# Kernel tuning notes

Hardware: AMD Instinct MI355X
Metric: run time of the kernel (lower is better)

## Reference

```python
import jax, jax.numpy as jnp
import numpy as np

B, G, K = 16, 5000, 256
NUM_CELLS, HID = 100, 64
STEPS, ALPHA = 10, 0.1


def setup_inputs() -> dict:
    key = jax.random.key(0)
    ks = jax.random.split(key, 10)
    ctl = jax.random.normal(ks[0], (B, G), dtype=jnp.float32)
    drug_targets = jax.random.uniform(ks[1], (B, G), dtype=jnp.float32)
    cell_idx = jax.random.randint(ks[2], (B,), 0, NUM_CELLS)
    drug_fp = jax.random.normal(ks[3], (B, 128), dtype=jnp.float32)
    # gene->module membership matrix (constructor constant M_gk)
    M = jax.random.uniform(ks[4], (G, K), dtype=jnp.float32)
    # module-module adjacency (constructor constant A_kk), column-normalized for stability
    A = jax.random.uniform(ks[5], (K, K), dtype=jnp.float32)
    A = A / jnp.sum(A, axis=0, keepdims=True)
    # shared Dense(hidden_dim, relu): input feature dim is 3 (ctl, t, z_gene stacked)
    W1 = jax.random.normal(ks[6], (3, HID), dtype=jnp.float32) * 0.5
    b1 = jnp.zeros((HID,), dtype=jnp.float32)
    cell_emb = jax.random.normal(ks[7], (NUM_CELLS, HID), dtype=jnp.float32) * 0.05
    W2 = jax.random.normal(ks[8], (HID, 1), dtype=jnp.float32) * 0.1
    b2 = jnp.zeros((1,), dtype=jnp.float32)
    return {"ctl": ctl, "drug_targets": drug_targets, "cell_idx": cell_idx,
            "drug_fp": drug_fp, "M": M, "A": A, "W1": W1, "b1": b1,
            "cell_emb": cell_emb, "W2": W2, "b2": b2}


def reference(ctl, drug_targets, cell_idx, drug_fp, M, A, W1, b1, cell_emb, W2, b2):
    t = drug_targets                                   # [B, G]
    # max-pool gene targets into modules: max_g t[b,g] * M[g,k]
    t_mod = jnp.max(t[:, :, None] * M[None, :, :], axis=1)   # [B, K]
    # APPNP propagation: Z = (1-alpha) * Z @ A + alpha * S, fixed 10 steps
    Z = t_mod
    for _ in range(STEPS):
        Z = (1.0 - ALPHA) * (Z @ A) + ALPHA * t_mod
    z_gene = Z @ M.T                                   # [B, G]
    x = jnp.stack([ctl, t, z_gene], axis=-1)           # [B, G, 3]
    h = jax.nn.relu(x @ W1 + b1)                       # [B, G, HID]
    h = h + cell_emb[cell_idx][:, None, :]             # broadcast cell embedding
    y = jnp.squeeze(h @ W2 + b2, axis=-1)              # [B, G]
    return y
```

## Files before the change

kernel.cpp:

```cpp
#include <hip/hip_runtime.h>

#define G 5000
#define K 256
#define BATCH 16
#define HID 64
#define STEPS 10
#define NC 125
#define GPER 40

__global__ void maxpool_kernel(const float* __restrict__ t,
                               const float* __restrict__ M,
                               float* __restrict__ partials) {
    __shared__ float4 tl[GPER];
    const int c   = blockIdx.x % NC;
    const int bg  = blockIdx.x / NC;
    const int tid = threadIdx.x;
    const int g0  = c * GPER;
    const int b0  = bg * 4;

    if (tid < GPER) {
        int g = g0 + tid;
        tl[tid] = make_float4(t[(b0 + 0) * G + g], t[(b0 + 1) * G + g],
                              t[(b0 + 2) * G + g], t[(b0 + 3) * G + g]);
    }
    __syncthreads();

    float mx0 = 0.f, mx1 = 0.f, mx2 = 0.f, mx3 = 0.f;
#pragma unroll 8
    for (int gi = 0; gi < GPER; ++gi) {
        float mg = M[(size_t)(g0 + gi) * K + tid];
        float4 tv = tl[gi];
        mx0 = fmaxf(mx0, tv.x * mg);
        mx1 = fmaxf(mx1, tv.y * mg);
        mx2 = fmaxf(mx2, tv.z * mg);
        mx3 = fmaxf(mx3, tv.w * mg);
    }
    partials[((size_t)c * BATCH + b0 + 0) * K + tid] = mx0;
    partials[((size_t)c * BATCH + b0 + 1) * K + tid] = mx1;
    partials[((size_t)c * BATCH + b0 + 2) * K + tid] = mx2;
    partials[((size_t)c * BATCH + b0 + 3) * K + tid] = mx3;
}

__global__ __launch_bounds__(1024)
void appnp_fused(const float* __restrict__ partials,
                 const float* __restrict__ A,
                 const int* __restrict__ cell_idx,
                 const float* __restrict__ cell_emb,
                 const float* __restrict__ W2,
                 const float* __restrict__ b2,
                 float* __restrict__ Zfin,
                 float* __restrict__ ce_dot) {
    __shared__ float As[56 * K];
    __shared__ float z0[K], z1[K], Sm[K];
    __shared__ float red[4][K];
    __shared__ float ce_red[HID];

    const int b  = blockIdx.x;
    const int t  = threadIdx.x;
    const int k  = t & 255;
    const int jc = t >> 8;

    const float4* A4  = (const float4*)A;
    float4*       As4 = (float4*)As;
    for (int i = t; i < 56 * K / 4; i += 1024) As4[i] = A4[i];

    {
        int c0 = jc * 32, c1 = min(NC, c0 + 32);
        float m = 0.f;
        for (int c = c0; c < c1; ++c)
            m = fmaxf(m, partials[((size_t)c * BATCH + b) * K + k]);
        red[jc][k] = m;
    }
    if (t < HID) {
        int ci = cell_idx[b];
        ce_red[t] = cell_emb[ci * HID + t] * W2[t];
    }
    __syncthreads();
    if (jc == 0) {
        float s = fmaxf(fmaxf(red[0][k], red[1][k]), fmaxf(red[2][k], red[3][k]));
        Sm[k] = s;
        z0[k] = s;
    }
    if (t == 0) {
        float s = b2[0];
        for (int h = 0; h < HID; ++h) s += ce_red[h];
        ce_dot[b] = s;
    }
    __syncthreads();

    for (int s = 0; s < STEPS; ++s) {
        const float* cur = (s & 1) ? z1 : z0;
        float*       nxt = (s & 1) ? z0 : z1;
        float acc = 0.f;
        if (jc == 0) {
#pragma unroll 8
            for (int j = 0; j < 56; ++j)
                acc = fmaf(cur[j], As[j * K + k], acc);
#pragma unroll
            for (int j = 56; j < 64; ++j)
                acc = fmaf(cur[j], A[(size_t)j * K + k], acc);
        } else {
            const int j0 = jc * 64;
#pragma unroll 8
            for (int j = j0; j < j0 + 64; ++j)
                acc = fmaf(cur[j], A[(size_t)j * K + k], acc);
        }
        red[jc][k] = acc;
        __syncthreads();
        if (jc == 0)
            nxt[k] = 0.9f * (red[0][k] + red[1][k] + red[2][k] + red[3][k])
                   + 0.1f * Sm[k];
        __syncthreads();
    }
    if (jc == 0) Zfin[b * K + k] = z0[k];
}

__global__ void final_kernel(const float* __restrict__ ctl,
                             const float* __restrict__ t_in,
                             const float* __restrict__ Z,
                             const float* __restrict__ M,
                             const float* __restrict__ W1,
                             const float* __restrict__ b1,
                             const float* __restrict__ W2,
                             const float* __restrict__ ce_dot,
                             float* __restrict__ out) {
    __shared__ float4 zl[BATCH * (K / 4)];
    __shared__ float4 wpack[HID];
    __shared__ float  w2l[HID];
    __shared__ float  cel[BATCH];

    const int t = threadIdx.x;
    const float4* Z4 = (const float4*)Z;
    for (int i = t; i < BATCH * (K / 4); i += 256) zl[i] = Z4[i];
    if (t < HID) {
        wpack[t] = make_float4(W1[t], W1[HID + t], W1[2 * HID + t], b1[t]);
        w2l[t] = W2[t];
    }
    if (t < BATCH) cel[t] = ce_dot[t];
    __syncthreads();

    const int gl = t & 63;
    const int bg = t >> 6;
    const int g = blockIdx.x * 64 + gl;
    if (g >= G) return;

    float acc[4] = {0.f, 0.f, 0.f, 0.f};
    const float4* M4 = (const float4*)(M + (size_t)g * K);
#pragma unroll 4
    for (int k4 = 0; k4 < K / 4; ++k4) {
        float4 m4 = M4[k4];
#pragma unroll
        for (int i = 0; i < 4; ++i) {
            float4 z4 = zl[(bg * 4 + i) * (K / 4) + k4];
            acc[i] = fmaf(m4.x, z4.x, acc[i]);
            acc[i] = fmaf(m4.y, z4.y, acc[i]);
            acc[i] = fmaf(m4.z, z4.z, acc[i]);
            acc[i] = fmaf(m4.w, z4.w, acc[i]);
        }
    }

    float cv[4], tv[4], y[4];
#pragma unroll
    for (int i = 0; i < 4; ++i) {
        int b = bg * 4 + i;
        cv[i] = ctl[b * G + g];
        tv[i] = t_in[b * G + g];
        y[i] = cel[b];
    }
#pragma unroll 4
    for (int h = 0; h < HID; ++h) {
        float4 w = wpack[h];
        float w2h = w2l[h];
#pragma unroll
        for (int i = 0; i < 4; ++i) {
            float pre = w.w;
            pre = fmaf(cv[i], w.x, pre);
            pre = fmaf(tv[i], w.y, pre);
            pre = fmaf(acc[i], w.z, pre);
            pre = fmaxf(pre, 0.f);
            y[i] = fmaf(pre, w2h, y[i]);
        }
    }
#pragma unroll
    for (int i = 0; i < 4; ++i)
        out[(bg * 4 + i) * G + g] = y[i];
}

extern "C" void kernel_launch(void* const* d_in, const int* in_sizes, int n_in,
                              void* d_out, int out_size, void* d_ws, size_t ws_size,
                              hipStream_t stream) {
    const float* ctl      = (const float*)d_in[0];
    const float* tgt      = (const float*)d_in[1];
    const int*   cell_idx = (const int*)d_in[2];
    const float* M        = (const float*)d_in[4];
    const float* A        = (const float*)d_in[5];
    const float* W1       = (const float*)d_in[6];
    const float* b1       = (const float*)d_in[7];
    const float* cell_emb = (const float*)d_in[8];
    const float* W2       = (const float*)d_in[9];
    const float* b2       = (const float*)d_in[10];
    float* out = (float*)d_out;

    float* partials = (float*)d_ws;
    float* Zfin = partials + (size_t)NC * BATCH * K;
    float* ce   = Zfin + BATCH * K;

    maxpool_kernel<<<NC * 4, 256, 0, stream>>>(tgt, M, partials);
    appnp_fused<<<BATCH, 1024, 0, stream>>>(partials, A, cell_idx, cell_emb,
                                            W2, b2, Zfin, ce);
    final_kernel<<<(G + 63) / 64, 256, 0, stream>>>(ctl, tgt, Zfin, M, W1, b1,
                                                    W2, ce, out);
}
```

Measured before the change: 126.2 us.

## Hold APPNP adjacency slices in registers and coarsen max-pool partials

The APPNP kernel now loads each thread's 64-entry column slice of A into registers once, instead of staging 56 rows in LDS and re-reading the remaining rows from global memory every step. The current Z vector is read from LDS as float4 broadcasts. Separately, the max-pool kernel now splits genes into 50 chunks of 100 instead of 125 chunks of 40, so there are fewer partials to reduce but fewer blocks available for parallelism. Holding 64 values per thread with 1024 threads per block raises register pressure and may cause spills.

```diff
diff --git a/kernel.cpp b/kernel.cpp
--- a/kernel.cpp
+++ b/kernel.cpp
@@ -5,8 +5,8 @@
 #define BATCH 16
 #define HID 64
 #define STEPS 10
-#define NC 125
-#define GPER 40
+#define NC 50
+#define GPER 100
 
 __global__ void maxpool_kernel(const float* __restrict__ t,
                                const float* __restrict__ M,
@@ -26,7 +26,7 @@
     __syncthreads();
 
     float mx0 = 0.f, mx1 = 0.f, mx2 = 0.f, mx3 = 0.f;
-#pragma unroll 8
+#pragma unroll 4
     for (int gi = 0; gi < GPER; ++gi) {
         float mg = M[(size_t)(g0 + gi) * K + tid];
         float4 tv = tl[gi];
@@ -41,7 +41,7 @@
     partials[((size_t)c * BATCH + b0 + 3) * K + tid] = mx3;
 }
 
-__global__ __launch_bounds__(1024)
+__global__ __launch_bounds__(1024, 4)
 void appnp_fused(const float* __restrict__ partials,
                  const float* __restrict__ A,
                  const int* __restrict__ cell_idx,
@@ -50,22 +50,24 @@
                  const float* __restrict__ b2,
                  float* __restrict__ Zfin,
                  float* __restrict__ ce_dot) {
-    __shared__ float As[56 * K];
-    __shared__ float z0[K], z1[K], Sm[K];
-    __shared__ float red[4][K];
-    __shared__ float ce_red[HID];
+    __shared__ float4 zb[2][K / 4];
+    __shared__ float  Sm[K];
+    __shared__ float  red[4][K];
+    __shared__ float  ce_red[HID];
 
     const int b  = blockIdx.x;
     const int t  = threadIdx.x;
     const int k  = t & 255;
     const int jc = t >> 8;
-
-    const float4* A4  = (const float4*)A;
-    float4*       As4 = (float4*)As;
-    for (int i = t; i < 56 * K / 4; i += 1024) As4[i] = A4[i];
+    const int j0 = jc * 64;
+
+    float Areg[64];
+#pragma unroll
+    for (int jj = 0; jj < 64; ++jj)
+        Areg[jj] = A[(size_t)(j0 + jj) * K + k];
 
     {
-        int c0 = jc * 32, c1 = min(NC, c0 + 32);
+        int c0 = jc * 13, c1 = min(NC, c0 + 13);
         float m = 0.f;
         for (int c = c0; c < c1; ++c)
             m = fmaxf(m, partials[((size_t)c * BATCH + b) * K + k]);
@@ -79,7 +81,7 @@
     if (jc == 0) {
         float s = fmaxf(fmaxf(red[0][k], red[1][k]), fmaxf(red[2][k], red[3][k]));
         Sm[k] = s;
-        z0[k] = s;
+        ((float*)zb)[k] = s;
     }
     if (t == 0) {
         float s = b2[0];
@@ -89,21 +91,16 @@
     __syncthreads();
 
     for (int s = 0; s < STEPS; ++s) {
-        const float* cur = (s & 1) ? z1 : z0;
-        float*       nxt = (s & 1) ? z0 : z1;
+        const float4* cur4 = zb[s & 1] + (j0 >> 2);
+        float*        nxt  = (float*)zb[(s + 1) & 1];
         float acc = 0.f;
-        if (jc == 0) {
-#pragma unroll 8
-            for (int j = 0; j < 56; ++j)
-                acc = fmaf(cur[j], As[j * K + k], acc);
-#pragma unroll
-            for (int j = 56; j < 64; ++j)
-                acc = fmaf(cur[j], A[(size_t)j * K + k], acc);
-        } else {
-            const int j0 = jc * 64;
-#pragma unroll 8
-            for (int j = j0; j < j0 + 64; ++j)
-                acc = fmaf(cur[j], A[(size_t)j * K + k], acc);
+#pragma unroll
+        for (int q = 0; q < 16; ++q) {
+            float4 c4 = cur4[q];
+            acc = fmaf(c4.x, Areg[4 * q + 0], acc);
+            acc = fmaf(c4.y, Areg[4 * q + 1], acc);
+            acc = fmaf(c4.z, Areg[4 * q + 2], acc);
+            acc = fmaf(c4.w, Areg[4 * q + 3], acc);
         }
         red[jc][k] = acc;
         __syncthreads();
@@ -112,7 +109,7 @@
                    + 0.1f * Sm[k];
         __syncthreads();
     }
-    if (jc == 0) Zfin[b * K + k] = z0[k];
+    if (jc == 0) Zfin[b * K + k] = ((float*)zb)[k];
 }
 
 __global__ void final_kernel(const float* __restrict__ ctl,
```

After: 117.2 us. 1.08x faster.
